# Kernel tuning notes

Hardware: AMD Instinct MI355X
Metric: run time of the kernel (lower is better)

Reference implementation:

```python
import jax, jax.numpy as jnp
import numpy as np

H = W = 2048        # voxel grid
P0 = 0.1            # occupancy density
EPS = 1e-5          # BatchNorm eps (torch default)


def _grid(rs, cs):
    g = np.full((H, W), -1, np.int64)
    g[rs, cs] = np.arange(rs.size)
    return g


def _conv_map(g, rs, cs, s):
    # kernel map for 3x3 conv at tensor stride s: offsets {-s,0,s}^2, -1 = missing neighbor
    maps = []
    for dr in (-s, 0, s):
        for dc in (-s, 0, s):
            r2, c2 = rs + dr, cs + dc
            ok = (r2 >= 0) & (r2 < H) & (c2 >= 0) & (c2 < W)
            m = np.full(rs.size, -1, np.int64)
            m[ok] = g[r2[ok], c2[ok]]
            maps.append(m)
    return np.stack(maps, 1)  # [N, 9]


def _pool_map(g, rs, cs, s):
    # 2x2 max pool stride 2 at tensor stride s: out coords = floor to multiples of 2s
    out = np.unique(np.stack([rs - rs % (2 * s), cs - cs % (2 * s)], 1), axis=0)
    maps = []
    for dr in (0, s):
        for dc in (0, s):
            r2, c2 = out[:, 0] + dr, out[:, 1] + dc
            ok = (r2 < H) & (c2 < W)
            m = np.full(out.shape[0], -1, np.int64)
            m[ok] = g[r2[ok], c2[ok]]
            maps.append(m)
    return out, np.stack(maps, 1)  # coords, [N_out, 4]


def _build_maps():
    rng = np.random.default_rng(0)
    n0 = int(H * W * P0)
    flat = rng.choice(H * W, size=n0, replace=False)
    flat.sort()
    rs0, cs0 = np.divmod(flat, W)
    g0 = _grid(rs0, cs0)
    nbr0 = _conv_map(g0, rs0, cs0, 1)
    c1, pmap1 = _pool_map(g0, rs0, cs0, 1)
    g1 = _grid(c1[:, 0], c1[:, 1])
    nbr1 = _conv_map(g1, c1[:, 0], c1[:, 1], 2)
    c2, pmap2 = _pool_map(g1, c1[:, 0], c1[:, 1], 2)
    return n0, nbr0, pmap1, nbr1, pmap2, c2.shape[0]


def setup_inputs() -> dict:
    n0, nbr0, pmap1, nbr1, pmap2, n2 = _build_maps()
    key = jax.random.key(0)
    k0, k1, k2, k3 = jax.random.split(key, 4)
    f0 = jax.random.normal(k0, (n0, 1), jnp.float32)
    W1 = jax.random.normal(k1, (9, 1, 8), jnp.float32) * 0.3
    W2 = jax.random.normal(k2, (9, 8, 16), jnp.float32) * 0.12
    Wfc = jax.random.normal(k3, (16, 2), jnp.float32) * 0.25
    return dict(
        f0=f0, W1=W1, b1=jnp.zeros((8,), jnp.float32),
        gamma1=jnp.ones((8,), jnp.float32), beta1=jnp.zeros((8,), jnp.float32),
        W2=W2, b2=jnp.zeros((16,), jnp.float32),
        gamma2=jnp.ones((16,), jnp.float32), beta2=jnp.zeros((16,), jnp.float32),
        Wfc=Wfc, bfc=jnp.zeros((2,), jnp.float32),
        nbr0=jnp.asarray(nbr0), pmap1=jnp.asarray(pmap1),
        nbr1=jnp.asarray(nbr1), pmap2=jnp.asarray(pmap2),
    )


def _sparse_conv(f, nbr, Wk, b):
    # gather-matmul-scatter: missing neighbors contribute zero
    n = f.shape[0]
    fpad = jnp.concatenate([f, jnp.zeros((1, f.shape[1]), f.dtype)], 0)
    g = fpad[jnp.where(nbr < 0, n, nbr)]  # [N_out, 9, C_in]
    return jnp.einsum('nkc,kcd->nd', g, Wk) + b


def _bn_relu(x, gamma, beta):
    mu = x.mean(0)
    var = x.var(0)  # biased, as torch BN normalization
    return jax.nn.relu((x - mu) * jax.lax.rsqrt(var + EPS) * gamma + beta)


def _max_pool(f, pmap):
    # max over existing children only (every output has >= 1 child)
    n = f.shape[0]
    fpad = jnp.concatenate([f, jnp.full((1, f.shape[1]), -jnp.inf, f.dtype)], 0)
    return fpad[jnp.where(pmap < 0, n, pmap)].max(1)


def reference(f0, W1, b1, gamma1, beta1, W2, b2, gamma2, beta2, Wfc, bfc,
              nbr0, pmap1, nbr1, pmap2):
    x = _bn_relu(_sparse_conv(f0, nbr0, W1, b1), gamma1, beta1)
    x = _max_pool(x, pmap1)
    x = _bn_relu(_sparse_conv(x, nbr1, W2, b2), gamma2, beta2)
    x = _max_pool(x, pmap2)
    return x @ Wfc + bfc
```

## Files before the change

kernel.cpp:

```cpp
#include <hip/hip_runtime.h>
#include <hip/hip_fp16.h>

#define EPS 1e-5f
#define NSLOT 64

__device__ __forceinline__ float waveReduceSum(float v) {
    #pragma unroll
    for (int off = 32; off > 0; off >>= 1)
        v += __shfl_down(v, off, 64);
    return v;
}

template <int NV>
__device__ __forceinline__ float statReduce(float (&v)[NV], int lane) {
    #pragma unroll
    for (int b = 0; (1 << b) < NV; ++b) {
        const int d = 1 << b;
        const bool hi = (lane >> b) & 1;
        #pragma unroll
        for (int i = 0; i < (NV >> (b + 1)); ++i) {
            float kept = hi ? v[2 * i + 1] : v[2 * i];
            float sent = hi ? v[2 * i] : v[2 * i + 1];
            float recv = __shfl_xor(sent, d, 64);
            v[i] = kept + recv;
        }
    }
    float r = v[0];
    #pragma unroll
    for (int d = NV; d < 64; d <<= 1)
        r += __shfl_xor(r, d, 64);
    return r;
}

__device__ __forceinline__ void unpack8(float4 raw, float* g) {
    const __half2* hp = reinterpret_cast<const __half2*>(&raw);
    #pragma unroll
    for (int q = 0; q < 4; ++q) {
        float2 f = __half22float2(hp[q]);
        g[2 * q] = f.x; g[2 * q + 1] = f.y;
    }
}

__device__ __forceinline__ float4 pack8(const float* g) {
    __half2 hp[4];
    #pragma unroll
    for (int q = 0; q < 4; ++q)
        hp[q] = __floats2half2_rn(g[2 * q], g[2 * q + 1]);
    return *reinterpret_cast<float4*>(hp);
}

__global__ __launch_bounds__(256) void k_zero(float4* __restrict__ slots,
                                              float4* __restrict__ p1zrow) {
    const float4 z4 = {0.f, 0.f, 0.f, 0.f};
    #pragma unroll
    for (int q = 0; q < 4; ++q)
        slots[q * 256 + threadIdx.x] = z4;
    if (threadIdx.x == 0) p1zrow[0] = z4;
}

__global__ __launch_bounds__(256, 4) void k_conv1(
        const float* __restrict__ f0, const float* __restrict__ W1,
        const float* __restrict__ b1, const int* __restrict__ nbr0,
        float4* __restrict__ x1h, float* __restrict__ slots, int n0) {
    __shared__ float sred[16];
    int t = threadIdx.x;
    int lane = t & 63;
    if (t < 16) sred[t] = 0.f;
    __syncthreads();

    int n = blockIdx.x * blockDim.x + t;
    bool valid = (n < n0);
    int nn = valid ? n : (n0 - 1);

    int idx[9];
    #pragma unroll
    for (int k = 0; k < 9; ++k) idx[k] = nbr0[(size_t)nn * 9 + k];
    float v[9];
    #pragma unroll
    for (int k = 0; k < 9; ++k) {
        float f = f0[idx[k] >= 0 ? idx[k] : 0];
        v[k] = (idx[k] >= 0) ? f : 0.f;
    }

    float acc[8];
    #pragma unroll
    for (int c = 0; c < 8; ++c) acc[c] = b1[c];
    #pragma unroll
    for (int k = 0; k < 9; ++k)
        #pragma unroll
        for (int c = 0; c < 8; ++c) acc[c] = fmaf(v[k], W1[k * 8 + c], acc[c]);

    if (valid) x1h[n] = pack8(acc);
    else {
        #pragma unroll
        for (int c = 0; c < 8; ++c) acc[c] = 0.f;
    }

    float red[16];
    #pragma unroll
    for (int c = 0; c < 8; ++c) {
        red[c] = acc[c];
        red[8 + c] = acc[c] * acc[c];
    }
    float tot = statReduce<16>(red, lane);
    if (lane < 16) atomicAdd(&sred[lane], tot);
    __syncthreads();
    if (t < 16)
        atomicAdd(&slots[(size_t)(blockIdx.x & (NSLOT - 1)) * 64 + t], sred[t]);
}

__global__ __launch_bounds__(64) void k_bn1stats(
        const float* __restrict__ slots, const float* __restrict__ gamma1,
        const float* __restrict__ beta1, float* __restrict__ stats, float invn0) {
    __shared__ float st[16];
    int t = threadIdx.x;
    if (t < 16) {
        float s = 0.f;
        #pragma unroll 8
        for (int k = 0; k < NSLOT; ++k) s += slots[(size_t)k * 64 + t];
        st[t] = s;
    }
    __syncthreads();
    if (t < 8) {
        float mu  = st[t] * invn0;
        float var = st[8 + t] * invn0 - mu * mu;
        float sc  = rsqrtf(var + EPS) * gamma1[t];
        stats[t]     = sc;
        stats[8 + t] = beta1[t] - sc * mu;
    }
}

__global__ __launch_bounds__(256, 4) void k_pool1(
        const float4* __restrict__ x1h, const int* __restrict__ pmap1,
        const float* __restrict__ stats, float4* __restrict__ p1h, int n1) {
    int i = blockIdx.x * blockDim.x + threadIdx.x;
    if (i >= n1) return;

    int4 pm = ((const int4*)pmap1)[i];
    int idx[4] = {pm.x, pm.y, pm.z, pm.w};
    float best[8];
    #pragma unroll
    for (int c = 0; c < 8; ++c) best[c] = 0.f;
    #pragma unroll
    for (int k = 0; k < 4; ++k) {
        float4 raw = x1h[idx[k] >= 0 ? idx[k] : 0];
        float v[8];
        unpack8(raw, v);
        #pragma unroll
        for (int c = 0; c < 8; ++c) {
            float z = fmaxf(fmaf(v[c], stats[c], stats[8 + c]), 0.f);
            z = (idx[k] >= 0) ? z : 0.f;
            best[c] = fmaxf(best[c], z);
        }
    }
    p1h[i] = pack8(best);
}

__global__ __launch_bounds__(256, 4) void k_conv2(
        const float4* __restrict__ p1h, const float* __restrict__ W2,
        const float* __restrict__ b2, const int* __restrict__ nbr1,
        float* __restrict__ x2, float* __restrict__ slots, int n1) {
    __shared__ float sred[32];
    int t = threadIdx.x;
    int lane = t & 63;
    if (t < 32) sred[t] = 0.f;
    __syncthreads();

    int n = blockIdx.x * blockDim.x + t;
    bool valid = (n < n1);
    int nn = valid ? n : (n1 - 1);

    int idx[9];
    #pragma unroll
    for (int k = 0; k < 9; ++k) {
        int j = nbr1[(size_t)nn * 9 + k];
        idx[k] = (j >= 0) ? j : n1;
    }

    float acc[16];
    #pragma unroll
    for (int c = 0; c < 16; ++c) acc[c] = b2[c];

    #pragma unroll
    for (int k = 0; k < 9; ++k) {
        float4 raw = p1h[idx[k]];
        float g[8];
        unpack8(raw, g);
        #pragma unroll
        for (int ci = 0; ci < 8; ++ci) {
            #pragma unroll
            for (int c = 0; c < 16; ++c)
                acc[c] = fmaf(g[ci], W2[(k * 8 + ci) * 16 + c], acc[c]);
        }
    }

    if (valid) {
        float4* dst = (float4*)(x2 + (size_t)n * 16);
        #pragma unroll
        for (int q4 = 0; q4 < 4; ++q4)
            dst[q4] = make_float4(acc[q4 * 4], acc[q4 * 4 + 1],
                                  acc[q4 * 4 + 2], acc[q4 * 4 + 3]);
    } else {
        #pragma unroll
        for (int c = 0; c < 16; ++c) acc[c] = 0.f;
    }

    float red[32];
    #pragma unroll
    for (int c = 0; c < 16; ++c) {
        red[c] = acc[c];
        red[16 + c] = acc[c] * acc[c];
    }
    float tot = statReduce<32>(red, lane);
    if (lane < 32) atomicAdd(&sred[lane], tot);
    __syncthreads();
    if (t < 32)
        atomicAdd(&slots[(size_t)(blockIdx.x & (NSLOT - 1)) * 64 + 16 + t], sred[t]);
}

__global__ __launch_bounds__(256) void k_pool2_fc(
        const float* __restrict__ x2, const int* __restrict__ pmap2,
        const float* __restrict__ slots, const float* __restrict__ gamma2,
        const float* __restrict__ beta2, const float* __restrict__ Wfc,
        const float* __restrict__ bfc, float* __restrict__ out,
        int n2, float invn) {
    __shared__ float sstat[32];
    int t = threadIdx.x;
    if (t < 64) {
        const float4* s4 = (const float4*)(slots + (size_t)t * 64 + 16);
        float vals[32];
        #pragma unroll
        for (int q = 0; q < 8; ++q) {
            float4 a = s4[q];
            vals[q * 4 + 0] = a.x; vals[q * 4 + 1] = a.y;
            vals[q * 4 + 2] = a.z; vals[q * 4 + 3] = a.w;
        }
        #pragma unroll
        for (int c = 0; c < 32; ++c) {
            float s = waveReduceSum(vals[c]);
            if (t == 0) sstat[c] = s;
        }
    }
    __syncthreads();

    int i = blockIdx.x * blockDim.x + t;
    if (i >= n2) return;

    float m[16], sc[16], bb[16];
    #pragma unroll
    for (int c = 0; c < 16; ++c) {
        float mu  = sstat[c] * invn;
        float var = sstat[16 + c] * invn - mu * mu;
        m[c]  = mu;
        sc[c] = rsqrtf(var + EPS) * gamma2[c];
        bb[c] = beta2[c];
    }

    int4 pm = ((const int4*)pmap2)[i];
    int idx[4] = {pm.x, pm.y, pm.z, pm.w};
    float best[16];
    #pragma unroll
    for (int c = 0; c < 16; ++c) best[c] = 0.f;
    #pragma unroll
    for (int k = 0; k < 4; ++k) {
        int j = idx[k] >= 0 ? idx[k] : 0;
        const float4* src = (const float4*)(x2 + (size_t)j * 16);
        #pragma unroll
        for (int q4 = 0; q4 < 4; ++q4) {
            float4 v4 = src[q4];
            float v[4] = {v4.x, v4.y, v4.z, v4.w};
            #pragma unroll
            for (int c = 0; c < 4; ++c) {
                int cc = q4 * 4 + c;
                float z = fmaxf(fmaf(v[c] - m[cc], sc[cc], bb[cc]), 0.f);
                z = (idx[k] >= 0) ? z : 0.f;
                best[cc] = fmaxf(best[cc], z);
            }
        }
    }
    float o0 = bfc[0], o1 = bfc[1];
    #pragma unroll
    for (int c = 0; c < 16; ++c) {
        o0 = fmaf(best[c], Wfc[c * 2 + 0], o0);
        o1 = fmaf(best[c], Wfc[c * 2 + 1], o1);
    }
    out[(size_t)i * 2 + 0] = o0;
    out[(size_t)i * 2 + 1] = o1;
}

extern "C" void kernel_launch(void* const* d_in, const int* in_sizes, int n_in,
                              void* d_out, int out_size, void* d_ws, size_t ws_size,
                              hipStream_t stream) {
    const float* f0     = (const float*)d_in[0];
    const float* W1     = (const float*)d_in[1];
    const float* b1     = (const float*)d_in[2];
    const float* gamma1 = (const float*)d_in[3];
    const float* beta1  = (const float*)d_in[4];
    const float* W2     = (const float*)d_in[5];
    const float* b2     = (const float*)d_in[6];
    const float* gamma2 = (const float*)d_in[7];
    const float* beta2  = (const float*)d_in[8];
    const float* Wfc    = (const float*)d_in[9];
    const float* bfc    = (const float*)d_in[10];
    const int*   nbr0   = (const int*)d_in[11];
    const int*   pmap1  = (const int*)d_in[12];
    const int*   nbr1   = (const int*)d_in[13];
    const int*   pmap2  = (const int*)d_in[14];

    const int n0 = in_sizes[0];
    const int n1 = in_sizes[12] / 4;
    const int n2 = in_sizes[14] / 4;

    float*  ws    = (float*)d_ws;
    float*  slots = ws;
    float*  stats = ws + (size_t)NSLOT * 64;
    float4* x1h   = (float4*)(stats + 16);
    float4* p1h   = x1h + n0;
    float*  x2    = (float*)(p1h + n1 + 1);

    const int B = 256;
    k_zero<<<1, B, 0, stream>>>((float4*)slots, p1h + n1);
    k_conv1<<<(n0 + B - 1) / B, B, 0, stream>>>(f0, W1, b1, nbr0, x1h, slots, n0);
    k_bn1stats<<<1, 64, 0, stream>>>(slots, gamma1, beta1, stats, 1.0f / (float)n0);
    k_pool1<<<(n1 + B - 1) / B, B, 0, stream>>>(x1h, pmap1, stats, p1h, n1);
    k_conv2<<<(n1 + B - 1) / B, B, 0, stream>>>(p1h, W2, b2, nbr1, x2, slots, n1);
    k_pool2_fc<<<(n2 + B - 1) / B, B, 0, stream>>>(x2, pmap2, slots, gamma2, beta2,
                                                   Wfc, bfc, (float*)d_out,
                                                   n2, 1.0f / (float)n1);
}
```

Measured before the change: 75.80 us.

## Fuse conv2 with max-pool2 via monotone BN trick, add XCD block swizzle

Conv2 now runs in pool2 order, with four threads per output site each computing one child. The quad is max-reduced (or min-reduced where gamma is negative) before BN, relying on BN+ReLU being monotone per channel, so only pooled rows are written instead of the full x2 tensor. BN2 stats move to a small dedicated kernel and the final kernel just applies the affine, ReLU and FC. Blocks are also remapped across the 8 XCDs for locality. The cost is an extra launch, plus idle lanes where children are missing, since the grid now covers 4*n2 threads.

```diff
diff --git a/kernel.cpp b/kernel.cpp
--- a/kernel.cpp
+++ b/kernel.cpp
@@ -3,6 +3,7 @@
 
 #define EPS 1e-5f
 #define NSLOT 64
+#define FLT_BIG 3.402823466e+38f
 
 __device__ __forceinline__ float waveReduceSum(float v) {
     #pragma unroll
@@ -156,24 +157,36 @@
     p1h[i] = pack8(best);
 }
 
-__global__ __launch_bounds__(256, 4) void k_conv2(
+__global__ __launch_bounds__(256, 4) void k_conv2pool(
         const float4* __restrict__ p1h, const float* __restrict__ W2,
         const float* __restrict__ b2, const int* __restrict__ nbr1,
-        float* __restrict__ x2, float* __restrict__ slots, int n1) {
+        const int* __restrict__ pmap2, const float* __restrict__ gamma2,
+        float* __restrict__ pm2, float* __restrict__ slots,
+        int n1, int n2, int nblk) {
     __shared__ float sred[32];
     int t = threadIdx.x;
     int lane = t & 63;
     if (t < 32) sred[t] = 0.f;
     __syncthreads();
 
-    int n = blockIdx.x * blockDim.x + t;
-    bool valid = (n < n1);
-    int nn = valid ? n : (n1 - 1);
+    int wg  = blockIdx.x;
+    int q   = nblk >> 3, r = nblk & 7;
+    int xcd = wg & 7, off = wg >> 3;
+    int swz = (xcd < r ? xcd * (q + 1) : r * (q + 1) + (xcd - r) * q) + off;
+
+    int gt   = swz * 256 + t;
+    int site = gt >> 2;
+    int ck   = gt & 3;
+    bool sv  = (site < n2);
+    int scl  = sv ? site : (n2 - 1);
+    int child = pmap2[(size_t)scl * 4 + ck];
+    bool cv  = sv && (child >= 0);
+    int row  = cv ? child : 0;
 
     int idx[9];
     #pragma unroll
     for (int k = 0; k < 9; ++k) {
-        int j = nbr1[(size_t)nn * 9 + k];
+        int j = nbr1[(size_t)row * 9 + k];
         idx[k] = (j >= 0) ? j : n1;
     }
 
@@ -194,95 +207,80 @@
         }
     }
 
-    if (valid) {
-        float4* dst = (float4*)(x2 + (size_t)n * 16);
-        #pragma unroll
-        for (int q4 = 0; q4 < 4; ++q4)
-            dst[q4] = make_float4(acc[q4 * 4], acc[q4 * 4 + 1],
-                                  acc[q4 * 4 + 2], acc[q4 * 4 + 3]);
-    } else {
-        #pragma unroll
-        for (int c = 0; c < 16; ++c) acc[c] = 0.f;
-    }
-
     float red[32];
     #pragma unroll
     for (int c = 0; c < 16; ++c) {
-        red[c] = acc[c];
-        red[16 + c] = acc[c] * acc[c];
+        float a = cv ? acc[c] : 0.f;
+        red[c] = a;
+        red[16 + c] = a * a;
     }
     float tot = statReduce<32>(red, lane);
     if (lane < 32) atomicAdd(&sred[lane], tot);
+
+    float pv[16];
+    #pragma unroll
+    for (int c = 0; c < 16; ++c) {
+        bool gp = (gamma2[c] >= 0.f);
+        float v = cv ? acc[c] : (gp ? -FLT_BIG : FLT_BIG);
+        float m1 = __shfl_xor(v, 1, 64);
+        v = gp ? fmaxf(v, m1) : fminf(v, m1);
+        float m2 = __shfl_xor(v, 2, 64);
+        v = gp ? fmaxf(v, m2) : fminf(v, m2);
+        pv[c] = v;
+    }
+    if (sv && ck == 0) {
+        float4* dst = (float4*)(pm2 + (size_t)site * 16);
+        #pragma unroll
+        for (int q4 = 0; q4 < 4; ++q4)
+            dst[q4] = make_float4(pv[q4 * 4], pv[q4 * 4 + 1],
+                                  pv[q4 * 4 + 2], pv[q4 * 4 + 3]);
+    }
+
     __syncthreads();
     if (t < 32)
         atomicAdd(&slots[(size_t)(blockIdx.x & (NSLOT - 1)) * 64 + 16 + t], sred[t]);
 }
 
-__global__ __launch_bounds__(256) void k_pool2_fc(
-        const float* __restrict__ x2, const int* __restrict__ pmap2,
+__global__ __launch_bounds__(64) void k_bn2stats(
         const float* __restrict__ slots, const float* __restrict__ gamma2,
-        const float* __restrict__ beta2, const float* __restrict__ Wfc,
-        const float* __restrict__ bfc, float* __restrict__ out,
-        int n2, float invn) {
-    __shared__ float sstat[32];
+        const float* __restrict__ beta2, float* __restrict__ stats, float invn1) {
+    __shared__ float st[32];
     int t = threadIdx.x;
-    if (t < 64) {
-        const float4* s4 = (const float4*)(slots + (size_t)t * 64 + 16);
-        float vals[32];
-        #pragma unroll
-        for (int q = 0; q < 8; ++q) {
-            float4 a = s4[q];
-            vals[q * 4 + 0] = a.x; vals[q * 4 + 1] = a.y;
-            vals[q * 4 + 2] = a.z; vals[q * 4 + 3] = a.w;
+    if (t < 32) {
+        float s = 0.f;
+        #pragma unroll 8
+        for (int k = 0; k < NSLOT; ++k) s += slots[(size_t)k * 64 + 16 + t];
+        st[t] = s;
+    }
+    __syncthreads();
+    if (t < 16) {
+        float mu  = st[t] * invn1;
+        float var = st[16 + t] * invn1 - mu * mu;
+        float sc  = rsqrtf(var + EPS) * gamma2[t];
+        stats[16 + t] = sc;
+        stats[32 + t] = beta2[t] - sc * mu;
+    }
+}
+
+__global__ __launch_bounds__(256) void k_bn2fc(
+        const float* __restrict__ pm2, const float* __restrict__ stats,
+        const float* __restrict__ Wfc, const float* __restrict__ bfc,
+        float* __restrict__ out, int n2) {
+    int i = blockIdx.x * blockDim.x + threadIdx.x;
+    if (i >= n2) return;
+    const float4* src = (const float4*)(pm2 + (size_t)i * 16);
+    float o0 = bfc[0], o1 = bfc[1];
+    #pragma unroll
+    for (int q4 = 0; q4 < 4; ++q4) {
+        float4 v4 = src[q4];
+        float v[4] = {v4.x, v4.y, v4.z, v4.w};
+        #pragma unroll
+        for (int c = 0; c < 4; ++c) {
+            int cc = q4 * 4 + c;
+            float z = fmaxf(fmaf(v[c], stats[16 + cc], stats[32 + cc]), 0.f);
+            o0 = fmaf(z, Wfc[cc * 2 + 0], o0);
+            o1 = fmaf(z, Wfc[cc * 2 + 1], o1);
         }
-        #pragma unroll
-        for (int c = 0; c < 32; ++c) {
-            float s = waveReduceSum(vals[c]);
-            if (t == 0) sstat[c] = s;
-        }
-    }
-    __syncthreads();
-
-    int i = blockIdx.x * blockDim.x + t;
-    if (i >= n2) return;
-
-    float m[16], sc[16], bb[16];
-    #pragma unroll
-    for (int c = 0; c < 16; ++c) {
-        float mu  = sstat[c] * invn;
-        float var = sstat[16 + c] * invn - mu * mu;
-        m[c]  = mu;
-        sc[c] = rsqrtf(var + EPS) * gamma2[c];
-        bb[c] = beta2[c];
-    }
-
-    int4 pm = ((const int4*)pmap2)[i];
-    int idx[4] = {pm.x, pm.y, pm.z, pm.w};
-    float best[16];
-    #pragma unroll
-    for (int c = 0; c < 16; ++c) best[c] = 0.f;
-    #pragma unroll
-    for (int k = 0; k < 4; ++k) {
-        int j = idx[k] >= 0 ? idx[k] : 0;
-        const float4* src = (const float4*)(x2 + (size_t)j * 16);
-        #pragma unroll
-        for (int q4 = 0; q4 < 4; ++q4) {
-            float4 v4 = src[q4];
-            float v[4] = {v4.x, v4.y, v4.z, v4.w};
-            #pragma unroll
-            for (int c = 0; c < 4; ++c) {
-                int cc = q4 * 4 + c;
-                float z = fmaxf(fmaf(v[c] - m[cc], sc[cc], bb[cc]), 0.f);
-                z = (idx[k] >= 0) ? z : 0.f;
-                best[cc] = fmaxf(best[cc], z);
-            }
-        }
-    }
-    float o0 = bfc[0], o1 = bfc[1];
-    #pragma unroll
-    for (int c = 0; c < 16; ++c) {
-        o0 = fmaf(best[c], Wfc[c * 2 + 0], o0);
-        o1 = fmaf(best[c], Wfc[c * 2 + 1], o1);
     }
     out[(size_t)i * 2 + 0] = o0;
     out[(size_t)i * 2 + 1] = o1;
@@ -314,17 +312,19 @@
     float*  ws    = (float*)d_ws;
     float*  slots = ws;
     float*  stats = ws + (size_t)NSLOT * 64;
-    float4* x1h   = (float4*)(stats + 16);
+    float4* x1h   = (float4*)(stats + 64);
     float4* p1h   = x1h + n0;
-    float*  x2    = (float*)(p1h + n1 + 1);
+    float*  pm2   = (float*)(p1h + n1 + 1);
 
     const int B = 256;
+    const int nblk2 = (n2 * 4 + B - 1) / B;
     k_zero<<<1, B, 0, stream>>>((float4*)slots, p1h + n1);
     k_conv1<<<(n0 + B - 1) / B, B, 0, stream>>>(f0, W1, b1, nbr0, x1h, slots, n0);
     k_bn1stats<<<1, 64, 0, stream>>>(slots, gamma1, beta1, stats, 1.0f / (float)n0);
     k_pool1<<<(n1 + B - 1) / B, B, 0, stream>>>(x1h, pmap1, stats, p1h, n1);
-    k_conv2<<<(n1 + B - 1) / B, B, 0, stream>>>(p1h, W2, b2, nbr1, x2, slots, n1);
-    k_pool2_fc<<<(n2 + B - 1) / B, B, 0, stream>>>(x2, pmap2, slots, gamma2, beta2,
-                                                   Wfc, bfc, (float*)d_out,
-                                                   n2, 1.0f / (float)n1);
-}
+    k_conv2pool<<<nblk2, B, 0, stream>>>(p1h, W2, b2, nbr1, pmap2, gamma2,
+                                         pm2, slots, n1, n2, nblk2);
+    k_bn2stats<<<1, 64, 0, stream>>>(slots, gamma2, beta2, stats, 1.0f / (float)n1);
+    k_bn2fc<<<(n2 + B - 1) / B, B, 0, stream>>>(pm2, stats, Wfc, bfc,
+                                                (float*)d_out, n2);
+}
```

New measurement: 76.40 us. No clear change (+0.8%).
